# Kernel optimization log

Measured on AMD Instinct MI355X. Metric: run time of the kernel, lower is better.

The kernel has to match this reference:

```python
import jax, jax.numpy as jnp
import numpy as np
from jax.scipy.special import gammaln, xlogy

B, N, DIM, H, DK, DV = 2, 2048, 1536, 8, 64, 64
NRPF = 192  # num_rel_pos_features, already divisible by 6


def get_positional_embed(n, feat):
    # Enformer positional basis: exponential, central-mask, gamma; then sign-antisymmetrized.
    nb = feat // 6  # num basis per class
    d = jnp.arange(-n + 1, n, dtype=jnp.float32)          # [2n-1]
    ad = jnp.abs(d)[:, None]                              # [2n-1, 1]
    # exponential decay features
    max_range = np.log(n) / np.log(2.0)
    half_life = 2.0 ** jnp.linspace(3.0, max_range, nb)
    e = jnp.exp(-np.log(2.0) / half_life * ad)
    # central mask features
    widths = 2.0 ** jnp.arange(1, nb + 1, dtype=jnp.float32) - 1.0
    c = (widths > ad).astype(jnp.float32)
    # gamma pdf features
    std = n / (2.0 * nb)
    mean = jnp.linspace(n / nb, float(n), nb)
    conc = (mean / std) ** 2
    rate = mean / (std ** 2)
    logp = xlogy(conc - 1.0, ad) - rate * ad - (gammaln(conc) - conc * jnp.log(rate))
    p = jnp.exp(logp) + 1e-8
    g = p / jnp.max(p)
    emb = jnp.concatenate([e, c, g], axis=-1)             # [2n-1, feat//2]
    return jnp.concatenate([emb, jnp.sign(d)[:, None] * emb], axis=-1)  # [2n-1, feat]


def relative_shift(x):
    # x: [b, h, i, 2i-1] -> [b, h, i, i]
    b, h, i, j = x.shape
    x = jnp.pad(x, ((0, 0), (0, 0), (0, 0), (1, 0)))      # [b,h,i,j+1]
    x = x.reshape(b, h, j + 1, i)[:, :, 1:, :]            # drop first 'row'
    x = x.reshape(b, h, i, j)
    return x[..., : (j + 2) // 2]                          # keep first i cols


def setup_inputs() -> dict:
    key = jax.random.key(0)
    ks = jax.random.split(key, 9)
    s = 0.02
    return {
        "x": jax.random.normal(ks[0], (B, N, DIM), jnp.float32),
        "Wq": jax.random.normal(ks[1], (DIM, H * DK), jnp.float32) * s,
        "Wk": jax.random.normal(ks[2], (DIM, H * DK), jnp.float32) * s,
        "Wv": jax.random.normal(ks[3], (DIM, H * DV), jnp.float32) * s,
        "Wo": jax.random.normal(ks[4], (H * DV, DIM), jnp.float32) * s,
        "bo": jnp.zeros((DIM,), jnp.float32),
        "Wrel": jax.random.normal(ks[5], (NRPF, H * DK), jnp.float32) * s,
        "rel_content_bias": jax.random.normal(ks[6], (1, H, 1, DK), jnp.float32),
        "rel_pos_bias": jax.random.normal(ks[7], (1, H, 1, DK), jnp.float32),
    }


def reference(x, Wq, Wk, Wv, Wo, bo, Wrel, rel_content_bias, rel_pos_bias):
    b, n, _ = x.shape
    scale = DK ** -0.5
    split = lambda t, d: t.reshape(b, n, H, d).transpose(0, 2, 1, 3)  # b h n d
    q = split(x @ Wq, DK) * scale
    k = split(x @ Wk, DK)
    v = split(x @ Wv, DV)
    content_logits = jnp.einsum('bhid,bhjd->bhij', q + rel_content_bias, k)
    pos = get_positional_embed(n, NRPF) @ Wrel               # [2n-1, H*DK]
    pos = pos.reshape(2 * n - 1, H, DK).transpose(1, 0, 2)   # h j d
    rel_logits = jnp.einsum('bhid,hjd->bhij', q + rel_pos_bias, pos)
    rel_logits = relative_shift(rel_logits)
    attn = jax.nn.softmax(content_logits + rel_logits, axis=-1)
    out = jnp.einsum('bhij,bhjd->bhid', attn, v)
    out = out.transpose(0, 2, 1, 3).reshape(b, n, H * DV)
    return out @ Wo + bo
```

## Files before the change

kernel.cpp:

```cpp
#include <hip/hip_runtime.h>
#include <stdint.h>
#include <cmath>

#define B_    2
#define N_    2048
#define DIM_  1536
#define H_    8
#define NPOS  (2*N_ - 1)
#define NB_   32

typedef __attribute__((ext_vector_type(8))) short short8;
typedef __attribute__((ext_vector_type(4))) float float4v;

__device__ __forceinline__ float bf2f(unsigned short u) {
    return __uint_as_float(((unsigned int)u) << 16);
}
__device__ __forceinline__ unsigned short f2bf(float f) {
    unsigned int u = __float_as_uint(f);
    u += 0x7FFFu + ((u >> 16) & 1u);
    return (unsigned short)(u >> 16);
}
__device__ __forceinline__ unsigned int pack2bf(float lo, float hi) {
    return (unsigned int)f2bf(lo) | ((unsigned int)f2bf(hi) << 16);
}
__device__ __forceinline__ float ldf(const void* p, int isF32, size_t idx) {
    return isF32 ? ((const float*)p)[idx] : bf2f(((const unsigned short*)p)[idx]);
}
__device__ __forceinline__ void gll16(const unsigned short* g, unsigned short* l) {
    __builtin_amdgcn_global_load_lds(
        (const __attribute__((address_space(1))) unsigned int*)g,
        (__attribute__((address_space(3))) unsigned int*)l, 16, 0, 0);
}

constexpr size_t OFF_FLAG = 0;
constexpr size_t OFF_POS  = 256;
constexpr size_t OFF_Q    = OFF_POS + (size_t)H_*4096*64*2;
constexpr size_t OFF_K    = OFF_Q   + (size_t)B_*H_*N_*64*2;
constexpr size_t OFF_V    = OFF_K   + (size_t)B_*H_*N_*64*2;
constexpr size_t OFF_WOT  = OFF_V   + (size_t)B_*H_*N_*64*2;
constexpr size_t OFF_XB   = OFF_WOT + (size_t)DIM_*512*2;
constexpr size_t OFF_AO   = OFF_XB;
constexpr size_t OFF_OP   = OFF_AO + (size_t)4096*512*2;
constexpr size_t OFF_LP   = OFF_OP + (size_t)3*16*32*4096*2;
constexpr size_t OFF_WT   = OFF_XB + (size_t)4096*DIM_*2;
static_assert(OFF_LP + (size_t)3*16*32*64*4 <= OFF_WT + (size_t)3*512*DIM_*2, "ws overflow");

__global__ __launch_bounds__(256) void detect_kernel(const unsigned short* __restrict__ x,
                                                     unsigned int* __restrict__ flags) {
    __shared__ int cnt[256];
    unsigned short u = x[2 * threadIdx.x];
    int e  = (u >> 7) & 0xFF;
    int ok = (u == 0) || (e >= 95 && e <= 140);
    cnt[threadIdx.x] = ok;
    __syncthreads();
    for (int s = 128; s > 0; s >>= 1) {
        if (threadIdx.x < s) cnt[threadIdx.x] += cnt[threadIdx.x + s];
        __syncthreads();
    }
    if (threadIdx.x == 0) flags[0] = (cnt[0] >= 192) ? 0u : 1u;
}

__global__ __launch_bounds__(256) void cvtx_kernel(const unsigned int* __restrict__ flags,
                                                   const void* __restrict__ x,
                                                   unsigned short* __restrict__ Xb) {
    const int f32 = (int)flags[0];
    const size_t total = (size_t)4096 * DIM_;
    size_t i = ((size_t)blockIdx.x * 256 + threadIdx.x) * 8;
    const size_t stride = (size_t)gridDim.x * 256 * 8;
    if (f32) {
        for (; i < total; i += stride) {
            float4v a = *reinterpret_cast<const float4v*>((const float*)x + i);
            float4v b = *reinterpret_cast<const float4v*>((const float*)x + i + 4);
            uint4 o;
            o.x = pack2bf(a[0], a[1]); o.y = pack2bf(a[2], a[3]);
            o.z = pack2bf(b[0], b[1]); o.w = pack2bf(b[2], b[3]);
            *reinterpret_cast<uint4*>(Xb + i) = o;
        }
    } else {
        for (; i < total; i += stride)
            *reinterpret_cast<uint4*>(Xb + i) =
                *reinterpret_cast<const uint4*>((const unsigned short*)x + i);
    }
}

__global__ __launch_bounds__(256) void cvtw_kernel(const unsigned int* __restrict__ flags,
                                                   const void* __restrict__ Wq, const void* __restrict__ Wk,
                                                   const void* __restrict__ Wv, const void* __restrict__ Wo,
                                                   unsigned short* __restrict__ Wt,
                                                   unsigned short* __restrict__ Wot) {
    __shared__ unsigned short tile[32][33];
    const int f32 = (int)flags[0];
    const int z = blockIdx.z;
    const void* src = z == 0 ? Wq : (z == 1 ? Wk : (z == 2 ? Wv : Wo));
    unsigned short* dst = (z < 3) ? (Wt + (size_t)z * 512 * DIM_) : Wot;
    const int R = (z < 3) ? DIM_ : 512;
    const int C = (z < 3) ? 512 : DIM_;
    const int x0 = ((z < 3) ? blockIdx.x : blockIdx.y) * 32;
    const int y0 = ((z < 3) ? blockIdx.y : blockIdx.x) * 32;
    const int tx = threadIdx.x & 31, ty = threadIdx.x >> 5;
#pragma unroll
    for (int i = 0; i < 4; ++i)
        tile[ty + i * 8][tx] = f2bf(ldf(src, f32, (size_t)(y0 + ty + i * 8) * C + x0 + tx));
    __syncthreads();
#pragma unroll
    for (int i = 0; i < 4; ++i)
        dst[(size_t)(x0 + ty + i * 8) * R + y0 + tx] = tile[tx][ty + i * 8];
}

__global__ __launch_bounds__(512) void posproj_kernel(double maxp,
                                                      const void* __restrict__ Wrel,
                                                      const unsigned int* __restrict__ flags,
                                                      unsigned short* __restrict__ posb) {
    __shared__ float eb[8 * 192];
    const int f32 = (int)flags[0];
    const int j0  = blockIdx.x * 8;
    const int c   = threadIdx.x;
    const double max_range = log((double)N_) / log(2.0);

    for (int u = c; u < 8 * 96; u += 512) {
        int rr = u / 96, f = u - rr * 96;
        int j = j0 + rr;
        float v = 0.f, sg = 0.f;
        if (j < NPOS) {
            int dd  = j - (N_ - 1);
            int adI = dd < 0 ? -dd : dd;
            double ad = (double)adI;
            double val;
            if (f < 32) {
                double t = 3.0 + (double)f * (max_range - 3.0) / 31.0;
                val = exp2(-ad / exp2(t));
            } else if (f < 64) {
                double width = exp2((double)(f - 31)) - 1.0;
                val = (width > ad) ? 1.0 : 0.0;
            } else {
                int g = f - 64;
                double mean = 64.0 * (g + 1);
                double conc = (mean / 32.0) * (mean / 32.0);
                double rate = mean / 1024.0;
                double pp = (adI == 0) ? 1e-8
                          : exp((conc - 1.0) * log(ad) - rate * ad - lgamma(conc) + conc * log(rate)) + 1e-8;
                val = pp / maxp;
            }
            v  = (float)val;
            sg = (dd > 0) ? 1.f : ((dd < 0) ? -1.f : 0.f);
        }
        eb[rr * 192 + f]      = v;
        eb[rr * 192 + 96 + f] = sg * v;
    }
    __syncthreads();

    float acc[8] = {0, 0, 0, 0, 0, 0, 0, 0};
#pragma unroll 4
    for (int k = 0; k < 192; ++k) {
        float w = ldf(Wrel, f32, (size_t)k * 512 + c);
#pragma unroll
        for (int rr = 0; rr < 8; ++rr) acc[rr] += eb[rr * 192 + k] * w;
    }
    int h = c >> 6, dcol = c & 63;
    for (int rr = 0; rr < 8; ++rr) {
        int j = j0 + rr;
        if (j < NPOS)
            posb[((size_t)h * 4096 + j) * 64 + dcol] = f2bf(acc[rr]);
    }
}

__device__ __forceinline__ void gemm64x128_core(const unsigned short* __restrict__ A,
                                                const unsigned short* __restrict__ Bt,
                                                int K, int row0, int col0,
                                                unsigned short* As, unsigned short* Bs,
                                                float4v acc[2][4]) {
    const int tid = threadIdx.x, lane = tid & 63, w = tid >> 6;
    const int l15 = lane & 15, q8 = (lane >> 4) * 8;
    const int mr0 = (w & 1) * 32, nc0 = (w >> 1) * 64;
    const int sr = lane >> 2, sc8 = (lane & 3) * 8;
    for (int k0 = 0; k0 < K; k0 += 32) {
        __syncthreads();
        gll16(&A [(size_t)(row0 + w * 16 + sr) * K + k0 + sc8],      &As[w * 512]);
        gll16(&Bt[(size_t)(col0 + w * 32 + sr) * K + k0 + sc8],      &Bs[w * 1024]);
        gll16(&Bt[(size_t)(col0 + w * 32 + 16 + sr) * K + k0 + sc8], &Bs[w * 1024 + 512]);
        __syncthreads();
        short8 a[2], b[4];
#pragma unroll
        for (int mi = 0; mi < 2; ++mi)
            a[mi] = *reinterpret_cast<const short8*>(&As[(mr0 + mi * 16 + l15) * 32 + q8]);
#pragma unroll
        for (int ni = 0; ni < 4; ++ni)
            b[ni] = *reinterpret_cast<const short8*>(&Bs[(nc0 + ni * 16 + l15) * 32 + q8]);
#pragma unroll
        for (int mi = 0; mi < 2; ++mi)
#pragma unroll
            for (int ni = 0; ni < 4; ++ni)
                acc[mi][ni] = __builtin_amdgcn_mfma_f32_16x16x32_bf16(a[mi], b[ni], acc[mi][ni], 0, 0, 0);
    }
}

__global__ __launch_bounds__(256) void qkv_kernel(const unsigned short* __restrict__ Xb,
                                                  const unsigned short* __restrict__ Wt,
                                                  unsigned short* __restrict__ qbuf,
                                                  unsigned short* __restrict__ kbuf,
                                                  unsigned short* __restrict__ vbuf) {
    __shared__ __align__(16) unsigned short As[64 * 32];
    __shared__ __align__(16) unsigned short Bs[128 * 32];
    const int row0 = blockIdx.y * 64, col0 = blockIdx.x * 128;
    float4v acc[2][4];
#pragma unroll
    for (int mi = 0; mi < 2; ++mi)
#pragma unroll
        for (int ni = 0; ni < 4; ++ni) acc[mi][ni] = (float4v){0.f, 0.f, 0.f, 0.f};
    gemm64x128_core(Xb, Wt, DIM_, row0, col0, As, Bs, acc);
    const int lane = threadIdx.x & 63, w = threadIdx.x >> 6;
    const int l15 = lane & 15, quad = lane >> 4;
    const int mr0 = (w & 1) * 32, nc0 = (w >> 1) * 64;
#pragma unroll
    for (int mi = 0; mi < 2; ++mi)
#pragma unroll
        for (int ni = 0; ni < 4; ++ni) {
            int n = col0 + nc0 + ni * 16 + l15;
            int mode = n >> 9, nn = n & 511;
            int hh = nn >> 6, dd = nn & 63;
            unsigned short* Obuf = mode == 0 ? qbuf : (mode == 1 ? kbuf : vbuf);
            float scale = (mode == 0) ? 0.125f : 1.0f;
#pragma unroll
            for (int r = 0; r < 4; ++r) {
                int m = row0 + mr0 + mi * 16 + quad * 4 + r;
                int bb = m >> 11, ii = m & 2047;
                Obuf[((size_t)(bb * 8 + hh) * N_ + ii) * 64 + dd] = f2bf(acc[mi][ni][r] * scale);
            }
        }
}

#define SLD 72
#define RST 66

__device__ __forceinline__ void stage64(const unsigned short* __restrict__ g,
                                        unsigned short* __restrict__ s, int tid) {
    int r = tid >> 2, d0 = (tid & 3) * 16;
    const uint4* p = reinterpret_cast<const uint4*>(g + (size_t)r * 64 + d0);
    *reinterpret_cast<uint4*>(&s[r * SLD + d0])     = p[0];
    *reinterpret_cast<uint4*>(&s[r * SLD + d0 + 8]) = p[1];
}

__global__ __launch_bounds__(256) void attn_kernel(const unsigned int* __restrict__ flags,
                                                   const unsigned short* __restrict__ qb,
                                                   const unsigned short* __restrict__ kb,
                                                   const unsigned short* __restrict__ vb,
                                                   const unsigned short* __restrict__ posb,
                                                   const void* __restrict__ rcb,
                                                   const void* __restrict__ rpb,
                                                   unsigned short* __restrict__ Opart,
                                                   float* __restrict__ lpart) {
    __shared__ __align__(16) unsigned short Ks[64 * SLD];
    __shared__ __align__(16) unsigned short Ps[64 * SLD];
    __shared__ __align__(16) unsigned short Vt[64 * SLD];
    __shared__ __align__(16) unsigned short Pp[64 * SLD];
    __shared__ __align__(8)  unsigned short Rb[128 * RST];

    const int f32 = (int)flags[0];
    const int tid = threadIdx.x;
    const int it = blockIdx.x, bh = blockIdx.y, z = blockIdx.z;
    const int h = bh & 7;
    const int i0 = it * 64;
    const size_t qoff = (size_t)bh * N_ * 64;
    const size_t poff = (size_t)h * 4096 * 64;
    const int lane = tid & 63, w = tid >> 6;
    const int l15 = lane & 15, quad = lane >> 4, q8 = quad * 8;
    const int m0 = w * 16 + quad * 4;

    short8 afc[2], afr[2];
#pragma unroll
    for (int kc = 0; kc < 2; ++kc) {
        uint4 qv = *reinterpret_cast<const uint4*>(
            &qb[qoff + (size_t)(i0 + w * 16 + l15) * 64 + kc * 32 + q8]);
        unsigned int uu[4] = {qv.x, qv.y, qv.z, qv.w};
        unsigned int cw[4], rw[4];
#pragma unroll
        for (int e = 0; e < 4; ++e) {
            int k = h * 64 + kc * 32 + q8 + 2 * e;
            float lo = __uint_as_float(uu[e] << 16);
            float hi = __uint_as_float(uu[e] & 0xffff0000u);
            cw[e] = pack2bf(lo + ldf(rcb, f32, k), hi + ldf(rcb, f32, k + 1));
            rw[e] = pack2bf(lo + ldf(rpb, f32, k), hi + ldf(rpb, f32, k + 1));
        }
        union { uint4 u; short8 s; } cv, rv2;
        cv.u  = (uint4){cw[0], cw[1], cw[2], cw[3]};
        rv2.u = (uint4){rw[0], rw[1], rw[2], rw[3]};
        afc[kc] = cv.s;
        afr[kc] = rv2.s;
    }

    float4v Oa[4];
#pragma unroll
    for (int nb = 0; nb < 4; ++nb) Oa[nb] = (float4v){0.f, 0.f, 0.f, 0.f};
    float lsum[4] = {0.f, 0.f, 0.f, 0.f};

    const int base0 = 1984 - i0;
    const int t0 = z * 11, t1 = (z == 2) ? 32 : (t0 + 11);

    {
        const int cs0 = base0 + t0 * 64;
        stage64(&posb[poff + (size_t)cs0 * 64], Ps, tid);
        __syncthreads();
        float4v R[4];
#pragma unroll
        for (int nb = 0; nb < 4; ++nb) R[nb] = (float4v){0.f, 0.f, 0.f, 0.f};
#pragma unroll
        for (int kc = 0; kc < 2; ++kc)
#pragma unroll
            for (int nb = 0; nb < 4; ++nb) {
                short8 pb = *reinterpret_cast<const short8*>(&Ps[(nb * 16 + l15) * SLD + kc * 32 + q8]);
                R[nb] = __builtin_amdgcn_mfma_f32_16x16x32_bf16(afr[kc], pb, R[nb], 0, 0, 0);
            }
        const int cb0 = cs0 & 127;
#pragma unroll
        for (int nb = 0; nb < 4; ++nb) {
            union { unsigned short us[4]; uint2 u2; } rv;
#pragma unroll
            for (int r = 0; r < 4; ++r) rv.us[r] = f2bf(R[nb][r]);
            *reinterpret_cast<uint2*>(&Rb[(size_t)(cb0 + nb * 16 + l15) * RST + m0]) = rv.u2;
        }
    }

    for (int jt = t0; jt < t1; ++jt) {
        const int j0 = jt * 64, basej = base0 + j0;
        __syncthreads();

        stage64(&kb[qoff + (size_t)j0 * 64], Ks, tid);
        stage64(&posb[poff + (size_t)(basej + 64) * 64], Ps, tid);
        {
            int jj = (tid & 31) * 2, dv = (tid >> 5) * 8;
            uint4 r0 = *reinterpret_cast<const uint4*>(&vb[qoff + (size_t)(j0 + jj) * 64 + dv]);
            uint4 r1 = *reinterpret_cast<const uint4*>(&vb[qoff + (size_t)(j0 + jj + 1) * 64 + dv]);
            const unsigned short* p0 = (const unsigned short*)&r0;
            const unsigned short* p1 = (const unsigned short*)&r1;
#pragma unroll
            for (int e = 0; e < 8; ++e) {
                unsigned int pk = (unsigned int)p0[e] | ((unsigned int)p1[e] << 16);
                *reinterpret_cast<unsigned int*>(&Vt[(dv + e) * SLD + jj]) = pk;
            }
        }
        __syncthreads();

        {
            float4v R[4];
#pragma unroll
            for (int nb = 0; nb < 4; ++nb) R[nb] = (float4v){0.f, 0.f, 0.f, 0.f};
#pragma unroll
            for (int kc = 0; kc < 2; ++kc)
#pragma unroll
                for (int nb = 0; nb < 4; ++nb) {
                    short8 pb = *reinterpret_cast<const short8*>(&Ps[(nb * 16 + l15) * SLD + kc * 32 + q8]);
                    R[nb] = __builtin_amdgcn_mfma_f32_16x16x32_bf16(afr[kc], pb, R[nb], 0, 0, 0);
                }
            const int cb0 = (basej + 64) & 127;
#pragma unroll
            for (int nb = 0; nb < 4; ++nb) {
                union { unsigned short us[4]; uint2 u2; } rv;
#pragma unroll
                for (int r = 0; r < 4; ++r) rv.us[r] = f2bf(R[nb][r]);
                *reinterpret_cast<uint2*>(&Rb[(size_t)(cb0 + nb * 16 + l15) * RST + m0]) = rv.u2;
            }
        }

        float4v Sacc[4];
#pragma unroll
        for (int nb = 0; nb < 4; ++nb) Sacc[nb] = (float4v){0.f, 0.f, 0.f, 0.f};
#pragma unroll
        for (int kc = 0; kc < 2; ++kc)
#pragma unroll
            for (int nb = 0; nb < 4; ++nb) {
                short8 kf = *reinterpret_cast<const short8*>(&Ks[(nb * 16 + l15) * SLD + kc * 32 + q8]);
                Sacc[nb] = __builtin_amdgcn_mfma_f32_16x16x32_bf16(afc[kc], kf, Sacc[nb], 0, 0, 0);
            }

#pragma unroll
        for (int nb = 0; nb < 4; ++nb) {
            const int jl = nb * 16 + l15;
#pragma unroll
            for (int r = 0; r < 4; ++r) {
                int t = basej + 63 + jl - (m0 + r);
                float s = Sacc[nb][r] + bf2f(Rb[(size_t)(t & 127) * RST + m0 + r]);
                float p = __expf(s);
                lsum[r] += p;
                Pp[(m0 + r) * SLD + jl] = f2bf(p);
            }
        }

#pragma unroll
        for (int kc = 0; kc < 2; ++kc) {
            short8 pf = *reinterpret_cast<const short8*>(&Pp[(w * 16 + l15) * SLD + kc * 32 + q8]);
#pragma unroll
            for (int nb = 0; nb < 4; ++nb) {
                short8 vf = *reinterpret_cast<const short8*>(&Vt[(nb * 16 + l15) * SLD + kc * 32 + q8]);
                Oa[nb] = __builtin_amdgcn_mfma_f32_16x16x32_bf16(pf, vf, Oa[nb], 0, 0, 0);
            }
        }
    }

#pragma unroll
    for (int r = 0; r < 4; ++r)
#pragma unroll
        for (int off = 1; off < 16; off <<= 1) lsum[r] += __shfl_xor(lsum[r], off);
    const size_t pslot = (size_t)(z * 16 + bh) * 32 + it;
    const size_t obase = pslot * 4096;
#pragma unroll
    for (int nb = 0; nb < 4; ++nb)
#pragma unroll
        for (int r = 0; r < 4; ++r)
            Opart[obase + (size_t)(m0 + r) * 64 + nb * 16 + l15] = f2bf(Oa[nb][r]);
    if (l15 == 0) {
#pragma unroll
        for (int r = 0; r < 4; ++r) lpart[pslot * 64 + m0 + r] = lsum[r];
    }
}

__global__ __launch_bounds__(256) void combine_kernel(const unsigned short* __restrict__ Opart,
                                                      const float* __restrict__ lpart,
                                                      unsigned short* __restrict__ ao) {
    const int it = blockIdx.x, bh = blockIdx.y;
    const int h = bh & 7, b = bh >> 3, i0 = it * 64;
    const int tid = threadIdx.x;
    const int row = tid >> 2, c0 = (tid & 3) * 16;
    float o[16];
#pragma unroll
    for (int e = 0; e < 16; ++e) o[e] = 0.f;
    float l = 0.f;
#pragma unroll
    for (int z = 0; z < 3; ++z) {
        const size_t pslot = (size_t)(z * 16 + bh) * 32 + it;
        const size_t ob = pslot * 4096 + (size_t)row * 64 + c0;
        uint4 a = *reinterpret_cast<const uint4*>(&Opart[ob]);
        uint4 b4 = *reinterpret_cast<const uint4*>(&Opart[ob + 8]);
        unsigned int uu[8] = {a.x, a.y, a.z, a.w, b4.x, b4.y, b4.z, b4.w};
#pragma unroll
        for (int e = 0; e < 8; ++e) {
            o[2 * e]     += __uint_as_float(uu[e] << 16);
            o[2 * e + 1] += __uint_as_float(uu[e] & 0xffff0000u);
        }
        l += lpart[pslot * 64 + row];
    }
    float inv = 1.0f / l;
    unsigned int ou[8];
#pragma unroll
    for (int e = 0; e < 8; ++e) ou[e] = pack2bf(o[2 * e] * inv, o[2 * e + 1] * inv);
    unsigned short* dst = &ao[((size_t)b * N_ + i0 + row) * 512 + h * 64 + c0];
    *reinterpret_cast<uint4*>(dst)     = (uint4){ou[0], ou[1], ou[2], ou[3]};
    *reinterpret_cast<uint4*>(dst + 8) = (uint4){ou[4], ou[5], ou[6], ou[7]};
}

__global__ __launch_bounds__(256) void outproj_kernel(const unsigned int* __restrict__ flags,
                                                      const unsigned short* __restrict__ AO,
                                                      const unsigned short* __restrict__ Wot,
                                                      const void* __restrict__ bo,
                                                      void* __restrict__ out) {
    __shared__ __align__(16) unsigned short As[64 * 32];
    __shared__ __align__(16) unsigned short Bs[128 * 32];
    const int f32 = (int)flags[0];
    const int row0 = blockIdx.y * 64, col0 = blockIdx.x * 128;
    float4v acc[2][4];
#pragma unroll
    for (int mi = 0; mi < 2; ++mi)
#pragma unroll
        for (int ni = 0; ni < 4; ++ni) acc[mi][ni] = (float4v){0.f, 0.f, 0.f, 0.f};
    gemm64x128_core(AO, Wot, 512, row0, col0, As, Bs, acc);
    const int lane = threadIdx.x & 63, w = threadIdx.x >> 6;
    const int l15 = lane & 15, quad = lane >> 4;
    const int mr0 = (w & 1) * 32, nc0 = (w >> 1) * 64;
#pragma unroll
    for (int mi = 0; mi < 2; ++mi)
#pragma unroll
        for (int ni = 0; ni < 4; ++ni) {
            int n = col0 + nc0 + ni * 16 + l15;
            float bias = ldf(bo, f32, n);
#pragma unroll
            for (int r = 0; r < 4; ++r) {
                int m = row0 + mr0 + mi * 16 + quad * 4 + r;
                float v = acc[mi][ni][r] + bias;
                if (f32) ((float*)out)[(size_t)m * DIM_ + n] = v;
                else     ((unsigned short*)out)[(size_t)m * DIM_ + n] = f2bf(v);
            }
        }
}

extern "C" void kernel_launch(void* const* d_in, const int* in_sizes, int n_in,
                              void* d_out, int out_size, void* d_ws, size_t ws_size,
                              hipStream_t stream) {
    const void* x    = d_in[0];
    const void* Wq   = d_in[1];
    const void* Wk   = d_in[2];
    const void* Wv   = d_in[3];
    const void* Wo   = d_in[4];
    const void* bo   = d_in[5];
    const void* Wrel = d_in[6];
    const void* rcb  = d_in[7];
    const void* rpb  = d_in[8];

    char* ws = (char*)d_ws;
    unsigned int*   flags = (unsigned int*)(ws + OFF_FLAG);
    unsigned short* posb  = (unsigned short*)(ws + OFF_POS);
    unsigned short* qbuf  = (unsigned short*)(ws + OFF_Q);
    unsigned short* kbuf  = (unsigned short*)(ws + OFF_K);
    unsigned short* vbuf  = (unsigned short*)(ws + OFF_V);
    unsigned short* Wot   = (unsigned short*)(ws + OFF_WOT);
    unsigned short* Xb    = (unsigned short*)(ws + OFF_XB);
    unsigned short* ao    = (unsigned short*)(ws + OFF_AO);
    unsigned short* Opart = (unsigned short*)(ws + OFF_OP);
    float*          lpart = (float*)(ws + OFF_LP);
    unsigned short* Wt    = (unsigned short*)(ws + OFF_WT);

    double maxp = 0.0;
    for (int g = 0; g < NB_; ++g) {
        double mean = 64.0 * (g + 1);
        double conc = (mean / 32.0) * (mean / 32.0);
        double rate = mean / 1024.0;
        double lgc  = std::lgamma(conc);
        double clr  = conc * std::log(rate);
        for (int ad = 1; ad < N_; ++ad) {
            double lp = (conc - 1.0) * std::log((double)ad) - rate * (double)ad - lgc + clr;
            double p  = std::exp(lp) + 1e-8;
            if (p > maxp) maxp = p;
        }
    }

    detect_kernel<<<dim3(1), dim3(256), 0, stream>>>((const unsigned short*)x, flags);
    cvtx_kernel<<<dim3(1024), dim3(256), 0, stream>>>(flags, x, Xb);
    cvtw_kernel<<<dim3(16, 48, 4), dim3(256), 0, stream>>>(flags, Wq, Wk, Wv, Wo, Wt, Wot);
    posproj_kernel<<<dim3(512), dim3(512), 0, stream>>>(maxp, Wrel, flags, posb);
    qkv_kernel<<<dim3(12, 64), dim3(256), 0, stream>>>(Xb, Wt, qbuf, kbuf, vbuf);
    attn_kernel<<<dim3(32, 16, 3), dim3(256), 0, stream>>>(flags, qbuf, kbuf, vbuf, posb, rcb, rpb, Opart, lpart);
    combine_kernel<<<dim3(32, 16), dim3(256), 0, stream>>>(Opart, lpart, ao);
    outproj_kernel<<<dim3(12, 64), dim3(256), 0, stream>>>(flags, ao, Wot, bo, d_out);
}
```

Before: 289.8 us.

## Prefetch K/pos/V tiles into registers and store V pre-transposed

```diff
diff --git a/kernel.cpp b/kernel.cpp
--- a/kernel.cpp
+++ b/kernel.cpp
@@ -111,7 +111,7 @@
                                                       const void* __restrict__ Wrel,
                                                       const unsigned int* __restrict__ flags,
                                                       unsigned short* __restrict__ posb) {
-    __shared__ float eb[8 * 192];
+    __shared__ __align__(16) float eb[8 * 192];
     const int f32 = (int)flags[0];
     const int j0  = blockIdx.x * 8;
     const int c   = threadIdx.x;
@@ -150,11 +150,19 @@
     __syncthreads();
 
     float acc[8] = {0, 0, 0, 0, 0, 0, 0, 0};
-#pragma unroll 4
-    for (int k = 0; k < 192; ++k) {
-        float w = ldf(Wrel, f32, (size_t)k * 512 + c);
-#pragma unroll
-        for (int rr = 0; rr < 8; ++rr) acc[rr] += eb[rr * 192 + k] * w;
+    for (int k = 0; k < 192; k += 4) {
+        float w0 = ldf(Wrel, f32, (size_t)(k + 0) * 512 + c);
+        float w1 = ldf(Wrel, f32, (size_t)(k + 1) * 512 + c);
+        float w2 = ldf(Wrel, f32, (size_t)(k + 2) * 512 + c);
+        float w3 = ldf(Wrel, f32, (size_t)(k + 3) * 512 + c);
+#pragma unroll
+        for (int rr = 0; rr < 8; ++rr) {
+            float4v e = *reinterpret_cast<const float4v*>(&eb[rr * 192 + k]);
+            acc[rr] += e[0] * w0;
+            acc[rr] += e[1] * w1;
+            acc[rr] += e[2] * w2;
+            acc[rr] += e[3] * w3;
+        }
     }
     int h = c >> 6, dcol = c & 63;
     for (int rr = 0; rr < 8; ++rr) {
@@ -218,19 +226,26 @@
             int n = col0 + nc0 + ni * 16 + l15;
             int mode = n >> 9, nn = n & 511;
             int hh = nn >> 6, dd = nn & 63;
-            unsigned short* Obuf = mode == 0 ? qbuf : (mode == 1 ? kbuf : vbuf);
-            float scale = (mode == 0) ? 0.125f : 1.0f;
-#pragma unroll
-            for (int r = 0; r < 4; ++r) {
-                int m = row0 + mr0 + mi * 16 + quad * 4 + r;
-                int bb = m >> 11, ii = m & 2047;
-                Obuf[((size_t)(bb * 8 + hh) * N_ + ii) * 64 + dd] = f2bf(acc[mi][ni][r] * scale);
+            int mb = row0 + mr0 + mi * 16 + quad * 4;
+            int bb = mb >> 11, ii = mb & 2047;
+            if (mode == 2) {
+                union { unsigned short us[4]; uint2 u2; } pk;
+#pragma unroll
+                for (int r = 0; r < 4; ++r) pk.us[r] = f2bf(acc[mi][ni][r]);
+                *reinterpret_cast<uint2*>(
+                    &vbuf[((size_t)(bb * 8 + hh) * 64 + dd) * 2048 + ii]) = pk.u2;
+            } else {
+                unsigned short* Obuf = (mode == 0) ? qbuf : kbuf;
+                float scale = (mode == 0) ? 0.125f : 1.0f;
+#pragma unroll
+                for (int r = 0; r < 4; ++r)
+                    Obuf[((size_t)(bb * 8 + hh) * N_ + ii + r) * 64 + dd] = f2bf(acc[mi][ni][r] * scale);
             }
         }
 }
 
 #define SLD 72
-#define RST 66
+#define RST 68
 
 __device__ __forceinline__ void stage64(const unsigned short* __restrict__ g,
                                         unsigned short* __restrict__ s, int tid) {
@@ -261,10 +276,12 @@
     const int h = bh & 7;
     const int i0 = it * 64;
     const size_t qoff = (size_t)bh * N_ * 64;
+    const size_t voff = (size_t)bh * 64 * 2048;
     const size_t poff = (size_t)h * 4096 * 64;
     const int lane = tid & 63, w = tid >> 6;
     const int l15 = lane & 15, quad = lane >> 4, q8 = quad * 8;
     const int m0 = w * 16 + quad * 4;
+    const int sr = tid >> 2, sc = (tid & 3) * 16;
 
     short8 afc[2], afr[2];
 #pragma unroll
@@ -295,11 +312,11 @@
 
     const int base0 = 1984 - i0;
     const int t0 = z * 11, t1 = (z == 2) ? 32 : (t0 + 11);
-
+    const int cs0 = base0 + t0 * 64;
+
+    stage64(&posb[poff + (size_t)cs0 * 64], Ps, tid);
+    __syncthreads();
     {
-        const int cs0 = base0 + t0 * 64;
-        stage64(&posb[poff + (size_t)cs0 * 64], Ps, tid);
-        __syncthreads();
         float4v R[4];
 #pragma unroll
         for (int nb = 0; nb < 4; ++nb) R[nb] = (float4v){0.f, 0.f, 0.f, 0.f};
@@ -310,35 +327,43 @@
                 short8 pb = *reinterpret_cast<const short8*>(&Ps[(nb * 16 + l15) * SLD + kc * 32 + q8]);
                 R[nb] = __builtin_amdgcn_mfma_f32_16x16x32_bf16(afr[kc], pb, R[nb], 0, 0, 0);
             }
-        const int cb0 = cs0 & 127;
 #pragma unroll
         for (int nb = 0; nb < 4; ++nb) {
-            union { unsigned short us[4]; uint2 u2; } rv;
-#pragma unroll
-            for (int r = 0; r < 4; ++r) rv.us[r] = f2bf(R[nb][r]);
-            *reinterpret_cast<uint2*>(&Rb[(size_t)(cb0 + nb * 16 + l15) * RST + m0]) = rv.u2;
-        }
-    }
+            int ta = cs0 + nb * 16 + l15;
+#pragma unroll
+            for (int r = 0; r < 4; ++r) {
+                int m = m0 + r;
+                Rb[(size_t)((ta + m) & 127) * RST + m] = f2bf(R[nb][r]);
+            }
+        }
+    }
+    __syncthreads();
+
+    stage64(&kb[qoff + (size_t)(t0 * 64) * 64], Ks, tid);
+    stage64(&posb[poff + (size_t)(cs0 + 64) * 64], Ps, tid);
+    {
+        const unsigned short* gv = &vb[voff + (size_t)sr * 2048 + t0 * 64 + sc];
+        *reinterpret_cast<uint4*>(&Vt[sr * SLD + sc])     = *reinterpret_cast<const uint4*>(gv);
+        *reinterpret_cast<uint4*>(&Vt[sr * SLD + sc + 8]) = *reinterpret_cast<const uint4*>(gv + 8);
+    }
+    __syncthreads();
 
     for (int jt = t0; jt < t1; ++jt) {
         const int j0 = jt * 64, basej = base0 + j0;
-        __syncthreads();
-
-        stage64(&kb[qoff + (size_t)j0 * 64], Ks, tid);
-        stage64(&posb[poff + (size_t)(basej + 64) * 64], Ps, tid);
-        {
-            int jj = (tid & 31) * 2, dv = (tid >> 5) * 8;
-            uint4 r0 = *reinterpret_cast<const uint4*>(&vb[qoff + (size_t)(j0 + jj) * 64 + dv]);
-            uint4 r1 = *reinterpret_cast<const uint4*>(&vb[qoff + (size_t)(j0 + jj + 1) * 64 + dv]);
-            const unsigned short* p0 = (const unsigned short*)&r0;
-            const unsigned short* p1 = (const unsigned short*)&r1;
-#pragma unroll
-            for (int e = 0; e < 8; ++e) {
-                unsigned int pk = (unsigned int)p0[e] | ((unsigned int)p1[e] << 16);
-                *reinterpret_cast<unsigned int*>(&Vt[(dv + e) * SLD + jj]) = pk;
-            }
-        }
-        __syncthreads();
+        const bool hasn = (jt + 1 < t1);
+
+        uint4 kr0, kr1, pr0, pr1, vr0, vr1;
+        if (hasn) {
+            const unsigned short* gk = &kb[qoff + (size_t)(j0 + 64 + sr) * 64 + sc];
+            kr0 = *reinterpret_cast<const uint4*>(gk);
+            kr1 = *reinterpret_cast<const uint4*>(gk + 8);
+            const unsigned short* gp = &posb[poff + (size_t)(basej + 128 + sr) * 64 + sc];
+            pr0 = *reinterpret_cast<const uint4*>(gp);
+            pr1 = *reinterpret_cast<const uint4*>(gp + 8);
+            const unsigned short* gv = &vb[voff + (size_t)sr * 2048 + j0 + 64 + sc];
+            vr0 = *reinterpret_cast<const uint4*>(gv);
+            vr1 = *reinterpret_cast<const uint4*>(gv + 8);
+        }
 
         {
             float4v R[4];
@@ -351,13 +376,15 @@
                     short8 pb = *reinterpret_cast<const short8*>(&Ps[(nb * 16 + l15) * SLD + kc * 32 + q8]);
                     R[nb] = __builtin_amdgcn_mfma_f32_16x16x32_bf16(afr[kc], pb, R[nb], 0, 0, 0);
                 }
-            const int cb0 = (basej + 64) & 127;
+            const int tb = basej + 64;
 #pragma unroll
             for (int nb = 0; nb < 4; ++nb) {
-                union { unsigned short us[4]; uint2 u2; } rv;
-#pragma unroll
-                for (int r = 0; r < 4; ++r) rv.us[r] = f2bf(R[nb][r]);
-                *reinterpret_cast<uint2*>(&Rb[(size_t)(cb0 + nb * 16 + l15) * RST + m0]) = rv.u2;
+                int ta = tb + nb * 16 + l15;
+#pragma unroll
+                for (int r = 0; r < 4; ++r) {
+                    int m = m0 + r;
+                    Rb[(size_t)((ta + m) & 127) * RST + m] = f2bf(R[nb][r]);
+                }
             }
         }
 
@@ -375,11 +402,12 @@
 #pragma unroll
         for (int nb = 0; nb < 4; ++nb) {
             const int jl = nb * 16 + l15;
+            const int row = (basej + 63 + jl) & 127;
+            union { uint2 u2; unsigned short us[4]; } rv;
+            rv.u2 = *reinterpret_cast<const uint2*>(&Rb[(size_t)row * RST + m0]);
 #pragma unroll
             for (int r = 0; r < 4; ++r) {
-                int t = basej + 63 + jl - (m0 + r);
-                float s = Sacc[nb][r] + bf2f(Rb[(size_t)(t & 127) * RST + m0 + r]);
-                float p = __expf(s);
+                float p = __expf(Sacc[nb][r] + bf2f(rv.us[r]));
                 lsum[r] += p;
                 Pp[(m0 + r) * SLD + jl] = f2bf(p);
             }
@@ -394,6 +422,17 @@
                 Oa[nb] = __builtin_amdgcn_mfma_f32_16x16x32_bf16(pf, vf, Oa[nb], 0, 0, 0);
             }
         }
+
+        if (hasn) {
+            __syncthreads();
+            *reinterpret_cast<uint4*>(&Ks[sr * SLD + sc])     = kr0;
+            *reinterpret_cast<uint4*>(&Ks[sr * SLD + sc + 8]) = kr1;
+            *reinterpret_cast<uint4*>(&Ps[sr * SLD + sc])     = pr0;
+            *reinterpret_cast<uint4*>(&Ps[sr * SLD + sc + 8]) = pr1;
+            *reinterpret_cast<uint4*>(&Vt[sr * SLD + sc])     = vr0;
+            *reinterpret_cast<uint4*>(&Vt[sr * SLD + sc + 8]) = vr1;
+            __syncthreads();
+        }
     }
 
 #pragma unroll
@@ -406,7 +445,14 @@
     for (int nb = 0; nb < 4; ++nb)
 #pragma unroll
         for (int r = 0; r < 4; ++r)
-            Opart[obase + (size_t)(m0 + r) * 64 + nb * 16 + l15] = f2bf(Oa[nb][r]);
+            Pp[(m0 + r) * SLD + nb * 16 + l15] = f2bf(Oa[nb][r]);
+    {
+        const int rr2 = w * 16 + (lane >> 2), cc2 = (lane & 3) * 16;
+        uint4 o0 = *reinterpret_cast<const uint4*>(&Pp[rr2 * SLD + cc2]);
+        uint4 o1 = *reinterpret_cast<const uint4*>(&Pp[rr2 * SLD + cc2 + 8]);
+        *reinterpret_cast<uint4*>(&Opart[obase + (size_t)rr2 * 64 + cc2])     = o0;
+        *reinterpret_cast<uint4*>(&Opart[obase + (size_t)rr2 * 64 + cc2 + 8]) = o1;
+    }
     if (l15 == 0) {
 #pragma unroll
         for (int r = 0; r < 4; ++r) lpart[pslot * 64 + m0 + r] = lsum[r];
```

Result: faster. 279.9 us (-3.4%).
